# Optimization experiments

Hardware: AMD Instinct MI355X
Metric: run time of the kernel (lower is better)

Reference implementation:

```python
import jax, jax.numpy as jnp
import numpy as np


def setup_inputs() -> dict:
    key = jax.random.key(0)
    k1, k2, k3 = jax.random.split(key, 3)
    B, C_in, C_out, T = 16, 512, 512, 4096
    pre = jax.random.normal(k1, (B, C_in, T), dtype=jnp.float32)
    # nn.Linear weight layout: [out_features, in_features]
    W_pre = jax.random.normal(k2, (C_out, C_in), dtype=jnp.float32) * (1.0 / np.sqrt(C_in))
    b_pre = jax.random.normal(k3, (C_out,), dtype=jnp.float32) * 0.01
    return {"pre": pre, "W_pre": W_pre, "b_pre": b_pre}


def reference(pre, W_pre, b_pre):
    # Original 'casual' branch loops over T applying w_pre(_pre[:,:,i]) into BOTH
    # embedding_prev and embedding_curr, then sums -> 2 * (W_pre @ pre + b).
    # Batched form: one einsum over the full sequence.
    y = jnp.einsum('bct,oc->bot', pre, W_pre) + b_pre[None, :, None]  # [B, C_out, T]
    return y + y
```

## Files before the change

kernel.cpp:

```cpp
#include <hip/hip_runtime.h>
#include <hip/hip_bf16.h>

typedef __attribute__((ext_vector_type(8))) short short8_t;
typedef __attribute__((ext_vector_type(4))) float f32x4;

#define BATCH 16
#define CIN   512
#define COUT  512
#define TT    4096
#define BKT   32
#define NKT   16

__device__ __forceinline__ uint pk2(float a, float b) {
    ushort lo = __builtin_bit_cast(ushort, __float2bfloat16(a));
    ushort hi = __builtin_bit_cast(ushort, __float2bfloat16(b));
    return (uint)lo | ((uint)hi << 16);
}

#define SCHEDB()    __builtin_amdgcn_sched_barrier(0)
#define WAIT_VM0()  do { asm volatile("s_waitcnt vmcnt(0)" ::: "memory"); SCHEDB(); } while (0)
#define WAIT_VM4()  do { asm volatile("s_waitcnt vmcnt(4)" ::: "memory"); SCHEDB(); } while (0)
#define WAIT_VM6()  do { asm volatile("s_waitcnt vmcnt(6)" ::: "memory"); SCHEDB(); } while (0)
#define WAIT_VM8()  do { asm volatile("s_waitcnt vmcnt(8)" ::: "memory"); SCHEDB(); } while (0)
#define WAIT_LGKM() do { asm volatile("s_waitcnt lgkmcnt(0)" ::: "memory"); SCHEDB(); } while (0)
#define RAW_BARRIER() do { __builtin_amdgcn_s_barrier(); SCHEDB(); } while (0)

extern "C" __global__ __launch_bounds__(256)
void wconv(const float* __restrict__ W, ushort* __restrict__ Wb)
{
    const int i  = blockIdx.x * 256 + threadIdx.x;
    const int m  = i >> 7;
    const int k0 = (i & 127) * 4;
    const float4 v = *(const float4*)(W + (size_t)m * CIN + k0);
    const int bm = m >> 4, r = m & 15;
    const int ksg = k0 >> 5, g = (k0 >> 3) & 3, k7 = k0 & 7;
    uint2 q;
    q.x = pk2(v.x, v.y);
    q.y = pk2(v.z, v.w);
    *(uint2*)&Wb[(size_t)bm * 8192 + ksg * 512 + g * 128 + r * 8 + k7] = q;
}

template<bool WSB>
__global__ __launch_bounds__(256)
void conv2x1_gemm(const float* __restrict__ pre, const float* __restrict__ W,
                  const ushort* __restrict__ Wb,
                  const float* __restrict__ bias, float* __restrict__ out)
{
    __shared__ float  RAW[4][BKT * 64];
    __shared__ ushort BF [2][4 * 64 * 8];

    const int tid  = threadIdx.x;
    const int lane = tid & 63;
    const int wv   = tid >> 6;
    const int g    = lane >> 4;
    const int l15  = lane & 15;

    const int id   = ((blockIdx.x & 7) << 8) | (blockIdx.x >> 3);
    const int mblk = id & 1;
    const int ti   = (id >> 1) & 63;
    const int bb   = id >> 7;

    const int m0 = mblk << 8;
    const int t0 = ti << 6;

    const float* preB   = pre + (size_t)bb * ((size_t)CIN * TT);
    const int    bmBase = (m0 >> 4) + wv * 4;

    f32x4 acc[4][4];
#pragma unroll
    for (int i = 0; i < 4; ++i)
#pragma unroll
        for (int j = 0; j < 4; ++j) acc[i][j] = (f32x4)0.0f;

    short8_t afA[4], afB[4];
    float    f[8];

#define STAGE(J) do { \
    _Pragma("unroll") \
    for (int i = 0; i < 2; ++i) { \
        const int krow = wv*8 + i*4 + (lane >> 4); \
        const float* gsrc = preB + (size_t)((J)*BKT + krow) * TT + t0 + ((lane & 15) << 2); \
        float* ldst = &RAW[(J) % 4][(wv*128 + i*64 + lane) * 4]; \
        __builtin_amdgcn_global_load_lds((const __attribute__((address_space(1))) void*)gsrc, \
                                         (__attribute__((address_space(3))) void*)ldst, 16, 0, 0); \
    } } while (0)

#define LOAD_A(KT, AF) do { \
    if constexpr (WSB) { \
        _Pragma("unroll") \
        for (int mi = 0; mi < 4; ++mi) \
            AF[mi] = *(const short8_t*)(Wb + (size_t)(bmBase + mi) * 8192 \
                                        + (KT) * 512 + g * 128 + l15 * 8); \
    } else { \
        _Pragma("unroll") \
        for (int mi = 0; mi < 4; ++mi) { \
            const float* ab = W + (size_t)(m0 + wv*64 + mi*16 + l15) * CIN + (KT)*BKT + g*8; \
            const float4 u0 = *(const float4*)ab; \
            const float4 u1 = *(const float4*)(ab + 4); \
            uint4 qq; \
            qq.x = pk2(u0.x, u0.y); qq.y = pk2(u0.z, u0.w); \
            qq.z = pk2(u1.x, u1.y); qq.w = pk2(u1.z, u1.w); \
            AF[mi] = __builtin_bit_cast(short8_t, qq); \
        } \
    } } while (0)

#define CVT_READ(J) do { \
    const int ct = tid & 63; \
    _Pragma("unroll") \
    for (int j = 0; j < 8; ++j) \
        f[j] = RAW[(J) % 4][(wv*8 + j) * 64 + ct]; \
    } while (0)

#define CVT_WRITE(J) do { \
    const int ct = tid & 63; \
    uint4 q; \
    q.x = pk2(f[0], f[1]); \
    q.y = pk2(f[2], f[3]); \
    q.z = pk2(f[4], f[5]); \
    q.w = pk2(f[6], f[7]); \
    *(uint4*)&BF[(J) & 1][wv * 512 + ct * 8] = q; \
    } while (0)

#define MFMA_STEP(J, AF) do { \
    __builtin_amdgcn_s_setprio(1); \
    short8_t bf[4]; \
    _Pragma("unroll") \
    for (int ni = 0; ni < 4; ++ni) \
        bf[ni] = *(const short8_t*)&BF[(J) & 1][g * 512 + (ni*16 + l15) * 8]; \
    _Pragma("unroll") \
    for (int mi = 0; mi < 4; ++mi) \
        _Pragma("unroll") \
        for (int ni = 0; ni < 4; ++ni) \
            acc[mi][ni] = __builtin_amdgcn_mfma_f32_16x16x32_bf16(AF[mi], bf[ni], acc[mi][ni], 0, 0, 0); \
    __builtin_amdgcn_s_setprio(0); \
    } while (0)

    STAGE(0);
    STAGE(1);
    STAGE(2);
    LOAD_A(0, afA);
    WAIT_VM8();
    RAW_BARRIER();
    CVT_READ(0);
    CVT_WRITE(0);

#pragma unroll
    for (int kt = 0; kt < NKT; ++kt) {
        if (kt + 1 < NKT) {
            if ((kt & 1) == 0) LOAD_A(kt + 1, afB);
            else               LOAD_A(kt + 1, afA);
        }
        if (kt + 3 < NKT) STAGE(kt + 3);
        if      (kt == 0)  WAIT_VM6();
        else if (kt <= 12) WAIT_VM8();
        else if (kt == 13) WAIT_VM6();
        else if (kt == 14) WAIT_VM4();
        else               WAIT_VM0();
        WAIT_LGKM();
        RAW_BARRIER();
        if (kt + 1 < NKT) CVT_READ(kt + 1);
        if ((kt & 1) == 0) MFMA_STEP(kt, afA);
        else               MFMA_STEP(kt, afB);
        if (kt + 1 < NKT) CVT_WRITE(kt + 1);
    }

    const int orow = m0 + wv*64 + g*4;
    float bv[4][4];
#pragma unroll
    for (int mi = 0; mi < 4; ++mi)
#pragma unroll
        for (int r = 0; r < 4; ++r)
            bv[mi][r] = bias[orow + mi*16 + r];

    float* outB = out + (size_t)bb * ((size_t)COUT * TT);
#pragma unroll
    for (int mi = 0; mi < 4; ++mi) {
#pragma unroll
        for (int ni = 0; ni < 4; ++ni) {
            const int t = t0 + ni*16 + l15;
#pragma unroll
            for (int r = 0; r < 4; ++r) {
                const int o = orow + mi*16 + r;
                outB[(size_t)o * TT + t] = 2.0f * (acc[mi][ni][r] + bv[mi][r]);
            }
        }
    }
}

extern "C" void kernel_launch(void* const* d_in, const int* in_sizes, int n_in,
                              void* d_out, int out_size, void* d_ws, size_t ws_size,
                              hipStream_t stream)
{
    const float* pre  = (const float*)d_in[0];
    const float* Wp   = (const float*)d_in[1];
    const float* bias = (const float*)d_in[2];
    float* out = (float*)d_out;

    const size_t wb_bytes = (size_t)COUT * CIN * sizeof(ushort);

    const dim3 grid(BATCH * 2 * 64);
    const dim3 block(256);

    if (ws_size >= wb_bytes) {
        ushort* Wb = (ushort*)d_ws;
        hipLaunchKernelGGL(wconv, dim3(256), dim3(256), 0, stream, Wp, Wb);
        hipLaunchKernelGGL((conv2x1_gemm<true>), grid, block, 0, stream,
                           pre, Wp, Wb, bias, out);
    } else {
        hipLaunchKernelGGL((conv2x1_gemm<false>), grid, block, 0, stream,
                           pre, Wp, (const ushort*)nullptr, bias, out);
    }
}
```

Baseline: 74.77 us.

## Double the time tile to 128 with 512-thread blocks sharing staged input

Blocks grow to 8 waves arranged 4 along output channels by 2 along time, so each block covers 256 outputs by 128 time steps and the grid is halved. The fp32-to-bf16 staged input tile is shared by both time-halves, and each weight fragment is reused over twice as many columns. In exchange the raw staging ring shrinks from 4 buffers to 3, so prefetch depth drops from three tiles ahead to two. The larger block also changes occupancy and register pressure per CU.

```diff
diff --git a/kernel.cpp b/kernel.cpp
--- a/kernel.cpp
+++ b/kernel.cpp
@@ -21,7 +21,6 @@
 #define WAIT_VM0()  do { asm volatile("s_waitcnt vmcnt(0)" ::: "memory"); SCHEDB(); } while (0)
 #define WAIT_VM4()  do { asm volatile("s_waitcnt vmcnt(4)" ::: "memory"); SCHEDB(); } while (0)
 #define WAIT_VM6()  do { asm volatile("s_waitcnt vmcnt(6)" ::: "memory"); SCHEDB(); } while (0)
-#define WAIT_VM8()  do { asm volatile("s_waitcnt vmcnt(8)" ::: "memory"); SCHEDB(); } while (0)
 #define WAIT_LGKM() do { asm volatile("s_waitcnt lgkmcnt(0)" ::: "memory"); SCHEDB(); } while (0)
 #define RAW_BARRIER() do { __builtin_amdgcn_s_barrier(); SCHEDB(); } while (0)
 
@@ -41,30 +40,32 @@
 }
 
 template<bool WSB>
-__global__ __launch_bounds__(256)
+__global__ __launch_bounds__(512)
 void conv2x1_gemm(const float* __restrict__ pre, const float* __restrict__ W,
                   const ushort* __restrict__ Wb,
                   const float* __restrict__ bias, float* __restrict__ out)
 {
-    __shared__ float  RAW[4][BKT * 64];
-    __shared__ ushort BF [2][4 * 64 * 8];
+    __shared__ float  RAW[3][BKT * 128];
+    __shared__ ushort BF [2][4 * 128 * 8];
 
     const int tid  = threadIdx.x;
     const int lane = tid & 63;
     const int wv   = tid >> 6;
+    const int wm   = wv >> 1;
+    const int wt   = wv & 1;
     const int g    = lane >> 4;
     const int l15  = lane & 15;
 
-    const int id   = ((blockIdx.x & 7) << 8) | (blockIdx.x >> 3);
+    const int id   = ((blockIdx.x & 7) << 7) | (blockIdx.x >> 3);
     const int mblk = id & 1;
-    const int ti   = (id >> 1) & 63;
-    const int bb   = id >> 7;
+    const int ti   = (id >> 1) & 31;
+    const int bb   = id >> 6;
 
     const int m0 = mblk << 8;
-    const int t0 = ti << 6;
+    const int t0 = ti << 7;
 
     const float* preB   = pre + (size_t)bb * ((size_t)CIN * TT);
-    const int    bmBase = (m0 >> 4) + wv * 4;
+    const int    bmBase = (m0 >> 4) + wm * 4;
 
     f32x4 acc[4][4];
 #pragma unroll
@@ -75,12 +76,17 @@
     short8_t afA[4], afB[4];
     float    f[8];
 
+    const int ct = tid & 127;
+    const int cp = tid >> 7;
+
 #define STAGE(J) do { \
     _Pragma("unroll") \
     for (int i = 0; i < 2; ++i) { \
-        const int krow = wv*8 + i*4 + (lane >> 4); \
-        const float* gsrc = preB + (size_t)((J)*BKT + krow) * TT + t0 + ((lane & 15) << 2); \
-        float* ldst = &RAW[(J) % 4][(wv*128 + i*64 + lane) * 4]; \
+        const int s  = i*512 + tid;           \
+        const int kr = s >> 5;                \
+        const int tc = (s & 31) << 2;         \
+        const float* gsrc = preB + (size_t)((J)*BKT + kr) * TT + t0 + tc; \
+        float* ldst = &RAW[(J) % 3][kr*128 + tc]; \
         __builtin_amdgcn_global_load_lds((const __attribute__((address_space(1))) void*)gsrc, \
                                          (__attribute__((address_space(3))) void*)ldst, 16, 0, 0); \
     } } while (0)
@@ -94,7 +100,7 @@
     } else { \
         _Pragma("unroll") \
         for (int mi = 0; mi < 4; ++mi) { \
-            const float* ab = W + (size_t)(m0 + wv*64 + mi*16 + l15) * CIN + (KT)*BKT + g*8; \
+            const float* ab = W + (size_t)(m0 + wm*64 + mi*16 + l15) * CIN + (KT)*BKT + g*8; \
             const float4 u0 = *(const float4*)ab; \
             const float4 u1 = *(const float4*)(ab + 4); \
             uint4 qq; \
@@ -105,20 +111,18 @@
     } } while (0)
 
 #define CVT_READ(J) do { \
-    const int ct = tid & 63; \
     _Pragma("unroll") \
     for (int j = 0; j < 8; ++j) \
-        f[j] = RAW[(J) % 4][(wv*8 + j) * 64 + ct]; \
+        f[j] = RAW[(J) % 3][(cp*8 + j) * 128 + ct]; \
     } while (0)
 
 #define CVT_WRITE(J) do { \
-    const int ct = tid & 63; \
     uint4 q; \
     q.x = pk2(f[0], f[1]); \
     q.y = pk2(f[2], f[3]); \
     q.z = pk2(f[4], f[5]); \
     q.w = pk2(f[6], f[7]); \
-    *(uint4*)&BF[(J) & 1][wv * 512 + ct * 8] = q; \
+    *(uint4*)&BF[(J) & 1][cp * 1024 + ct * 8] = q; \
     } while (0)
 
 #define MFMA_STEP(J, AF) do { \
@@ -126,7 +130,7 @@
     short8_t bf[4]; \
     _Pragma("unroll") \
     for (int ni = 0; ni < 4; ++ni) \
-        bf[ni] = *(const short8_t*)&BF[(J) & 1][g * 512 + (ni*16 + l15) * 8]; \
+        bf[ni] = *(const short8_t*)&BF[(J) & 1][g * 1024 + (wt*64 + ni*16 + l15) * 8]; \
     _Pragma("unroll") \
     for (int mi = 0; mi < 4; ++mi) \
         _Pragma("unroll") \
@@ -137,9 +141,8 @@
 
     STAGE(0);
     STAGE(1);
-    STAGE(2);
     LOAD_A(0, afA);
-    WAIT_VM8();
+    WAIT_VM6();
     RAW_BARRIER();
     CVT_READ(0);
     CVT_WRITE(0);
@@ -150,12 +153,10 @@
             if ((kt & 1) == 0) LOAD_A(kt + 1, afB);
             else               LOAD_A(kt + 1, afA);
         }
-        if (kt + 3 < NKT) STAGE(kt + 3);
-        if      (kt == 0)  WAIT_VM6();
-        else if (kt <= 12) WAIT_VM8();
-        else if (kt == 13) WAIT_VM6();
-        else if (kt == 14) WAIT_VM4();
-        else               WAIT_VM0();
+        if (kt + 2 < NKT) STAGE(kt + 2);
+        if      (kt + 2 < NKT) WAIT_VM6();
+        else if (kt + 1 < NKT) WAIT_VM4();
+        else                   WAIT_VM0();
         WAIT_LGKM();
         RAW_BARRIER();
         if (kt + 1 < NKT) CVT_READ(kt + 1);
@@ -164,7 +165,7 @@
         if (kt + 1 < NKT) CVT_WRITE(kt + 1);
     }
 
-    const int orow = m0 + wv*64 + g*4;
+    const int orow = m0 + wm*64 + g*4;
     float bv[4][4];
 #pragma unroll
     for (int mi = 0; mi < 4; ++mi)
@@ -177,7 +178,7 @@
     for (int mi = 0; mi < 4; ++mi) {
 #pragma unroll
         for (int ni = 0; ni < 4; ++ni) {
-            const int t = t0 + ni*16 + l15;
+            const int t = t0 + wt*64 + ni*16 + l15;
 #pragma unroll
             for (int r = 0; r < 4; ++r) {
                 const int o = orow + mi*16 + r;
@@ -198,8 +199,8 @@
 
     const size_t wb_bytes = (size_t)COUT * CIN * sizeof(ushort);
 
-    const dim3 grid(BATCH * 2 * 64);
-    const dim3 block(256);
+    const dim3 grid(BATCH * 2 * 32);
+    const dim3 block(512);
 
     if (ws_size >= wb_bytes) {
         ushort* Wb = (ushort*)d_ws;
```

After: 77.03 us. +3.0%, slower.
